# Performance work log

Hardware: AMD Instinct MI355X
Metric: run time of the kernel (lower is better)

## Reference

```python
import jax, jax.numpy as jnp
import numpy as np

N = 50000      # nodes
E = 800000     # edges (before self-loops)
F_IN = 128     # input features
HID = 64       # hidden width
CLS = 40       # classes
NEG_SLOPE = 0.2  # PyG GATConv default
EPS = 1e-16


def setup_inputs() -> dict:
    key = jax.random.key(0)
    ks = jax.random.split(key, 16)

    def lin(k, fi, fo):
        return jax.random.normal(k, (fi, fo), jnp.float32) / np.float32(np.sqrt(fi))

    def att(k, f):
        return jax.random.normal(k, (f,), jnp.float32) / np.float32(np.sqrt(f))

    return {
        "x": jax.random.normal(ks[0], (N, F_IN), jnp.float32),
        "edge_index": jax.random.randint(ks[1], (2, E), 0, N, dtype=jnp.int64),
        "W1": lin(ks[2], F_IN, HID), "a_src1": att(ks[3], HID), "a_dst1": att(ks[4], HID), "b1": jnp.zeros((HID,), jnp.float32),
        "W2": lin(ks[5], HID, HID),  "a_src2": att(ks[6], HID), "a_dst2": att(ks[7], HID), "b2": jnp.zeros((HID,), jnp.float32),
        "W3": lin(ks[8], HID, CLS),  "a_src3": att(ks[9], CLS), "a_dst3": att(ks[10], CLS), "b3": jnp.zeros((CLS,), jnp.float32),
    }


def gat_layer(x, src, dst, W, a_src, a_dst, b, n):
    # Single-head GATConv (PyG semantics, heads=1, add_self_loops already applied).
    h = x @ W                                  # [n, out]
    s_src = h @ a_src                          # [n]
    s_dst = h @ a_dst                          # [n]
    e = jax.nn.leaky_relu(s_src[src] + s_dst[dst], NEG_SLOPE)  # [E']
    # softmax over incoming edges of each destination node
    m = jax.ops.segment_max(e, dst, num_segments=n)            # [n]
    e = jnp.exp(e - m[dst])
    denom = jax.ops.segment_sum(e, dst, num_segments=n)        # [n]
    alpha = e / (denom[dst] + EPS)                             # [E']
    out = jax.ops.segment_sum(h[src] * alpha[:, None], dst, num_segments=n)
    return out + b


def reference(x, edge_index, W1, a_src1, a_dst1, b1, W2, a_src2, a_dst2, b2, W3, a_src3, a_dst3, b3):
    n = x.shape[0]
    loop = jnp.arange(n, dtype=edge_index.dtype)
    src = jnp.concatenate([edge_index[0], loop])   # add self-loops (GATConv default)
    dst = jnp.concatenate([edge_index[1], loop])

    h = gat_layer(x, src, dst, W1, a_src1, a_dst1, b1, n)
    h = jax.nn.gelu(h, approximate=False)          # torch F.gelu default = exact erf
    h = gat_layer(h, src, dst, W2, a_src2, a_dst2, b2, n)
    h = jax.nn.gelu(h, approximate=False)
    out = gat_layer(h, src, dst, W3, a_src3, a_dst3, b3, n)
    return out
```

## Files before the change

kernel.cpp:

```cpp
#include <hip/hip_runtime.h>
#include <hip/hip_bf16.h>
#include <math.h>


#define PAD_CAP 64
#define SCAT_BLOCKS 128

__device__ __forceinline__ int detect64(const int* __restrict__ ei) {
  int any = 0;
#pragma unroll
  for (int i = 1; i < 64; i += 2) any |= ei[i];
  return any == 0;
}

__device__ __forceinline__ void load_edge(const int* __restrict__ ei, int E,
                                          int e, int is64, int n, int& s,
                                          int& d) {
  if (is64) {
    s = ei[2 * e];
    d = ei[2 * (E + e)];
  } else {
    s = ei[e];
    d = ei[E + e];
  }
  s = min(max(s, 0), n - 1);
  d = min(max(d, 0), n - 1);
}


template <int F_IN, int F_OUT, bool SCATTER>
__global__ __launch_bounds__(256) void gemm_att(
    const float* __restrict__ x, const float* __restrict__ W,
    const float* __restrict__ a_src, const float* __restrict__ a_dst,
    __hip_bfloat16* __restrict__ h, float* __restrict__ s_src,
    float* __restrict__ s_dst, int n, const int* __restrict__ ei, int E,
    int* __restrict__ deg, int* __restrict__ col) {
  if constexpr (SCATTER) {
    if (blockIdx.x < SCAT_BLOCKS) {
      const int is64 = detect64(ei);
      const int total = E + n;
      const int stride = SCAT_BLOCKS * 256;
      int e = blockIdx.x * 256 + threadIdx.x;
      while (e < total) {
        int sv[8], dv[8], va[8], pos[8];
#pragma unroll
        for (int j = 0; j < 8; ++j) {
          const int ee = e + j * stride;
          va[j] = (ee < total);
          int s = 0, d = 0;
          if (va[j]) {
            if (ee < E) load_edge(ei, E, ee, is64, n, s, d);
            else { s = ee - E; d = ee - E; }
          }
          sv[j] = s;
          dv[j] = d;
        }
#pragma unroll
        for (int j = 0; j < 8; ++j)
          pos[j] = va[j] ? atomicAdd(deg + dv[j], 1) : PAD_CAP;
#pragma unroll
        for (int j = 0; j < 8; ++j)
          if (va[j] && pos[j] < PAD_CAP)
            col[((size_t)dv[j] << 6) + pos[j]] = sv[j];
        e += 8 * stride;
      }
      return;
    }
  }

  constexpr int TF = F_OUT / 4;
  __shared__ float Xt[F_IN * 65];
  __shared__ float red[2][4][64];
  const int wave = threadIdx.x >> 6, lane = threadIdx.x & 63;
  const int bid = SCATTER ? (int)blockIdx.x - SCAT_BLOCKS : (int)blockIdx.x;
  const int nb0 = bid * 64;
  const int node = nb0 + lane;

  {
    constexpr int Q = F_IN / 4;
    for (int i = threadIdx.x; i < 64 * Q; i += 256) {
      const int nd = i / Q, k4 = i % Q;
      float4 v = {0.f, 0.f, 0.f, 0.f};
      if (nb0 + nd < n)
        v = *(const float4*)(x + (size_t)(nb0 + nd) * F_IN + 4 * k4);
      Xt[(4 * k4 + 0) * 65 + nd] = v.x;
      Xt[(4 * k4 + 1) * 65 + nd] = v.y;
      Xt[(4 * k4 + 2) * 65 + nd] = v.z;
      Xt[(4 * k4 + 3) * 65 + nd] = v.w;
    }
  }
  __syncthreads();

  const int f0 = __builtin_amdgcn_readfirstlane(wave * TF);
  float acc[TF];
#pragma unroll
  for (int ff = 0; ff < TF; ++ff) acc[ff] = 0.f;

#pragma unroll 4
  for (int k = 0; k < F_IN; ++k) {
    const float xk = Xt[k * 65 + lane];
#pragma unroll
    for (int ff = 0; ff < TF; ++ff)
      acc[ff] = fmaf(xk, W[k * F_OUT + f0 + ff], acc[ff]);
  }

  float pa = 0.f, pb = 0.f;
#pragma unroll
  for (int ff = 0; ff < TF; ++ff) {
    pa = fmaf(acc[ff], a_src[f0 + ff], pa);
    pb = fmaf(acc[ff], a_dst[f0 + ff], pb);
  }
  if (node < n) {
#pragma unroll
    for (int ff = 0; ff < TF; ++ff)
      h[(size_t)node * F_OUT + f0 + ff] = __float2bfloat16(acc[ff]);
  }
  red[0][wave][lane] = pa;
  red[1][wave][lane] = pb;
  __syncthreads();
  if (wave == 0 && node < n) {
    s_src[node] = red[0][0][lane] + red[0][1][lane] + red[0][2][lane] +
                  red[0][3][lane];
    s_dst[node] = red[1][0][lane] + red[1][1][lane] + red[1][2][lane] +
                  red[1][3][lane];
  }
}

template <int F_OUT, bool GELU>
__global__ __launch_bounds__(256) void attn_aggr(
    const int* __restrict__ col, const int* __restrict__ deg_arr,
    const float* __restrict__ ssrc, const float* __restrict__ sdst,
    const __hip_bfloat16* __restrict__ h, const float* __restrict__ bias,
    float* __restrict__ out, int n) {
  constexpr int NF4 = (F_OUT + 3) / 4;
  const int wave = threadIdx.x >> 6, lane = threadIdx.x & 63;
  const int d = blockIdx.x * 4 + wave;
  if (d >= n) return;
  const int beg = d << 6;
  const int deg = min(deg_arr[d], PAD_CAP);
  const float sd = sdst[d];

  int s0 = 0;
  float w0 = 0.f;
  if (lane < deg) {
    s0 = col[beg + lane];
    float t = ssrc[s0] + sd;
    t = t > 0.f ? t : 0.2f * t;
    w0 = __expf(t);
  }
  float den = w0;
#pragma unroll
  for (int off = 32; off > 0; off >>= 1) den += __shfl_xor(den, off);
  const float inv = 1.f / (den + 1e-16f);

  const int q = lane >> 4, t4 = lane & 15;
  const bool act = (t4 < NF4);
  const unsigned short* __restrict__ hu = (const unsigned short*)h + 4 * t4;

  float ax = 0.f, ay = 0.f, az = 0.f, aw = 0.f;
  int i = 0;
  for (; i + 16 <= deg; i += 16) {
    int ss[4];
    float ww[4];
    uint2 hv[4];
#pragma unroll
    for (int j = 0; j < 4; ++j) {
      ss[j] = __shfl(s0, i + 4 * j + q);
      ww[j] = __shfl(w0, i + 4 * j + q);
    }
#pragma unroll
    for (int j = 0; j < 4; ++j) {
      hv[j].x = 0u;
      hv[j].y = 0u;
      if (act) hv[j] = *(const uint2*)(hu + (size_t)ss[j] * F_OUT);
    }
#pragma unroll
    for (int j = 0; j < 4; ++j) {
      ax = fmaf(ww[j], __uint_as_float(hv[j].x << 16), ax);
      ay = fmaf(ww[j], __uint_as_float(hv[j].x & 0xffff0000u), ay);
      az = fmaf(ww[j], __uint_as_float(hv[j].y << 16), az);
      aw = fmaf(ww[j], __uint_as_float(hv[j].y & 0xffff0000u), aw);
    }
  }
  for (; i < deg; i += 4) {
    const int ss = __shfl(s0, i + q);
    const float ww = __shfl(w0, i + q);
    uint2 hv;
    hv.x = 0u;
    hv.y = 0u;
    if (act) hv = *(const uint2*)(hu + (size_t)ss * F_OUT);
    ax = fmaf(ww, __uint_as_float(hv.x << 16), ax);
    ay = fmaf(ww, __uint_as_float(hv.x & 0xffff0000u), ay);
    az = fmaf(ww, __uint_as_float(hv.y << 16), az);
    aw = fmaf(ww, __uint_as_float(hv.y & 0xffff0000u), aw);
  }

#pragma unroll
  for (int off = 32; off >= 16; off >>= 1) {
    ax += __shfl_xor(ax, off);
    ay += __shfl_xor(ay, off);
    az += __shfl_xor(az, off);
    aw += __shfl_xor(aw, off);
  }

  if (lane < NF4) {
    const float4 bv = *(const float4*)(bias + 4 * lane);
    float r0 = ax * inv + bv.x;
    float r1 = ay * inv + bv.y;
    float r2 = az * inv + bv.z;
    float r3 = aw * inv + bv.w;
    if (GELU) {
      r0 = 0.5f * r0 * (1.f + erff(r0 * 0.70710678118654752f));
      r1 = 0.5f * r1 * (1.f + erff(r1 * 0.70710678118654752f));
      r2 = 0.5f * r2 * (1.f + erff(r2 * 0.70710678118654752f));
      r3 = 0.5f * r3 * (1.f + erff(r3 * 0.70710678118654752f));
    }
    *(float4*)(out + (size_t)d * F_OUT + 4 * lane) =
        make_float4(r0, r1, r2, r3);
  }
}

extern "C" void kernel_launch(void* const* d_in, const int* in_sizes, int n_in,
                              void* d_out, int out_size, void* d_ws,
                              size_t ws_size, hipStream_t stream) {
  const float* x = (const float*)d_in[0];
  const int* ei = (const int*)d_in[1];
  const float* W1 = (const float*)d_in[2];
  const float* as1 = (const float*)d_in[3];
  const float* ad1 = (const float*)d_in[4];
  const float* b1 = (const float*)d_in[5];
  const float* W2 = (const float*)d_in[6];
  const float* as2 = (const float*)d_in[7];
  const float* ad2 = (const float*)d_in[8];
  const float* b2 = (const float*)d_in[9];
  const float* W3 = (const float*)d_in[10];
  const float* as3 = (const float*)d_in[11];
  const float* ad3 = (const float*)d_in[12];
  const float* b3 = (const float*)d_in[13];

  const int n = in_sizes[0] / 128;
  const int E = in_sizes[1] / 2;

  const size_t need = ((size_t)n * (32 + 64 + 1 + 1 + 1 + PAD_CAP)) * 4 + 256;
  if (ws_size < need) return;

  __hip_bfloat16* hb = (__hip_bfloat16*)d_ws;
  float* B = (float*)d_ws + (size_t)n * 32;
  float* ssrc = B + (size_t)n * 64;
  float* sdst = ssrc + n;
  int* deg = (int*)(sdst + n);
  int* col = deg + n;

  const int gemm_blocks = (n + 63) / 64;
  const int aggr_blocks = (n + 3) / 4;

  hipMemsetAsync(deg, 0, (size_t)n * 4, stream);
  gemm_att<128, 64, true><<<gemm_blocks + SCAT_BLOCKS, 256, 0, stream>>>(
      x, W1, as1, ad1, hb, ssrc, sdst, n, ei, E, deg, col);
  attn_aggr<64, true><<<aggr_blocks, 256, 0, stream>>>(col, deg, ssrc, sdst,
                                                       hb, b1, B, n);

  gemm_att<64, 64, false><<<gemm_blocks, 256, 0, stream>>>(
      B, W2, as2, ad2, hb, ssrc, sdst, n, nullptr, 0, nullptr, nullptr);
  attn_aggr<64, true><<<aggr_blocks, 256, 0, stream>>>(col, deg, ssrc, sdst,
                                                       hb, b2, B, n);

  gemm_att<64, 40, false><<<gemm_blocks, 256, 0, stream>>>(
      B, W3, as3, ad3, hb, ssrc, sdst, n, nullptr, 0, nullptr, nullptr);
  attn_aggr<40, false><<<aggr_blocks, 256, 0, stream>>>(
      col, deg, ssrc, sdst, hb, b3, (float*)d_out, n);
}
```

Before: 252.9 us.

## Fuse attention aggregation with next layer's GEMM into one kernel

Adds an aggr_gemm kernel that runs the softmax-weighted neighbor aggregation plus bias and GELU for 64 destination nodes, stages the result in shared memory, then multiplies by the next layer's weights and computes the attention scores. This replaces separate attn_aggr and gemm_att launches for layers 1→2 and 2→3, removing the fp32 intermediate buffer round-trip through global memory and two launches. Ping-pong bf16 and score buffers avoid read/write hazards. The cost is 1024-thread blocks where each wave handles four nodes serially, which may reduce latency hiding for the gather, and the GEMM phase leaves some waves idle for F_OUT=40.

```diff
diff --git a/kernel.cpp b/kernel.cpp
--- a/kernel.cpp
+++ b/kernel.cpp
@@ -123,6 +123,144 @@
                   red[0][3][lane];
     s_dst[node] = red[1][0][lane] + red[1][1][lane] + red[1][2][lane] +
                   red[1][3][lane];
+  }
+}
+
+template <int F_OUT>
+__global__ __launch_bounds__(1024) void aggr_gemm(
+    const int* __restrict__ col, const int* __restrict__ deg_arr,
+    const float* __restrict__ ssrc, const float* __restrict__ sdst,
+    const __hip_bfloat16* __restrict__ h_in, const float* __restrict__ bias_in,
+    const float* __restrict__ W, const float* __restrict__ a_src,
+    const float* __restrict__ a_dst, __hip_bfloat16* __restrict__ h_out,
+    float* __restrict__ ssrc_out, float* __restrict__ sdst_out, int n) {
+  constexpr int F_IN = 64;
+  constexpr int NW = F_OUT / 4;
+  __shared__ float Xt[F_IN * 65];
+  __shared__ float red[2][16][64];
+  const int wave = threadIdx.x >> 6, lane = threadIdx.x & 63;
+  const int q = lane >> 4, t4 = lane & 15;
+  const int nb0 = blockIdx.x * 64;
+
+  float4 bv = make_float4(0.f, 0.f, 0.f, 0.f);
+  if (lane < 16) bv = *(const float4*)(bias_in + 4 * lane);
+
+  const unsigned short* __restrict__ hu = (const unsigned short*)h_in + 4 * t4;
+
+  for (int r = 0; r < 4; ++r) {
+    const int dl = 4 * wave + r;
+    const int d = nb0 + dl;
+    float ax = 0.f, ay = 0.f, az = 0.f, aw_ = 0.f, inv = 0.f;
+    if (d < n) {
+      const int beg = d << 6;
+      const int deg = min(deg_arr[d], PAD_CAP);
+      const float sd = sdst[d];
+      int s0 = 0;
+      float w0 = 0.f;
+      if (lane < deg) {
+        s0 = col[beg + lane];
+        float t = ssrc[s0] + sd;
+        t = t > 0.f ? t : 0.2f * t;
+        w0 = __expf(t);
+      }
+      float den = w0;
+#pragma unroll
+      for (int off = 32; off > 0; off >>= 1) den += __shfl_xor(den, off);
+      inv = 1.f / (den + 1e-16f);
+
+      int i = 0;
+      for (; i + 16 <= deg; i += 16) {
+        int ss[4];
+        float ww[4];
+        uint2 hv[4];
+#pragma unroll
+        for (int j = 0; j < 4; ++j) {
+          ss[j] = __shfl(s0, i + 4 * j + q);
+          ww[j] = __shfl(w0, i + 4 * j + q);
+        }
+#pragma unroll
+        for (int j = 0; j < 4; ++j)
+          hv[j] = *(const uint2*)(hu + (size_t)ss[j] * F_IN);
+#pragma unroll
+        for (int j = 0; j < 4; ++j) {
+          ax = fmaf(ww[j], __uint_as_float(hv[j].x << 16), ax);
+          ay = fmaf(ww[j], __uint_as_float(hv[j].x & 0xffff0000u), ay);
+          az = fmaf(ww[j], __uint_as_float(hv[j].y << 16), az);
+          aw_ = fmaf(ww[j], __uint_as_float(hv[j].y & 0xffff0000u), aw_);
+        }
+      }
+      for (; i < deg; i += 4) {
+        const int ss = __shfl(s0, i + q);
+        const float ww = __shfl(w0, i + q);
+        const uint2 hv = *(const uint2*)(hu + (size_t)ss * F_IN);
+        ax = fmaf(ww, __uint_as_float(hv.x << 16), ax);
+        ay = fmaf(ww, __uint_as_float(hv.x & 0xffff0000u), ay);
+        az = fmaf(ww, __uint_as_float(hv.y << 16), az);
+        aw_ = fmaf(ww, __uint_as_float(hv.y & 0xffff0000u), aw_);
+      }
+#pragma unroll
+      for (int off = 32; off >= 16; off >>= 1) {
+        ax += __shfl_xor(ax, off);
+        ay += __shfl_xor(ay, off);
+        az += __shfl_xor(az, off);
+        aw_ += __shfl_xor(aw_, off);
+      }
+    }
+    if (lane < 16) {
+      float r0 = 0.f, r1 = 0.f, r2 = 0.f, r3 = 0.f;
+      if (d < n) {
+        r0 = ax * inv + bv.x;
+        r1 = ay * inv + bv.y;
+        r2 = az * inv + bv.z;
+        r3 = aw_ * inv + bv.w;
+        r0 = 0.5f * r0 * (1.f + erff(r0 * 0.70710678118654752f));
+        r1 = 0.5f * r1 * (1.f + erff(r1 * 0.70710678118654752f));
+        r2 = 0.5f * r2 * (1.f + erff(r2 * 0.70710678118654752f));
+        r3 = 0.5f * r3 * (1.f + erff(r3 * 0.70710678118654752f));
+      }
+      Xt[(4 * lane + 0) * 65 + dl] = r0;
+      Xt[(4 * lane + 1) * 65 + dl] = r1;
+      Xt[(4 * lane + 2) * 65 + dl] = r2;
+      Xt[(4 * lane + 3) * 65 + dl] = r3;
+    }
+  }
+  __syncthreads();
+
+  float pa = 0.f, pb = 0.f;
+  const int node = nb0 + lane;
+  if (wave < NW) {
+    const int f0 = __builtin_amdgcn_readfirstlane(wave * 4);
+    float acc[4] = {0.f, 0.f, 0.f, 0.f};
+#pragma unroll 4
+    for (int k = 0; k < F_IN; ++k) {
+      const float xk = Xt[k * 65 + lane];
+#pragma unroll
+      for (int ff = 0; ff < 4; ++ff)
+        acc[ff] = fmaf(xk, W[k * F_OUT + f0 + ff], acc[ff]);
+    }
+#pragma unroll
+    for (int ff = 0; ff < 4; ++ff) {
+      pa = fmaf(acc[ff], a_src[f0 + ff], pa);
+      pb = fmaf(acc[ff], a_dst[f0 + ff], pb);
+    }
+    if (node < n) {
+#pragma unroll
+      for (int ff = 0; ff < 4; ++ff)
+        h_out[(size_t)node * F_OUT + f0 + ff] = __float2bfloat16(acc[ff]);
+    }
+  }
+  red[0][wave][lane] = pa;
+  red[1][wave][lane] = pb;
+  __syncthreads();
+  if (wave == 0 && node < n) {
+    float sa = 0.f, sb = 0.f;
+#pragma unroll
+    for (int w = 0; w < NW; ++w) {
+      sa += red[0][w][lane];
+      sb += red[1][w][lane];
+    }
+    ssrc_out[node] = sa;
+    sdst_out[node] = sb;
   }
 }
 
@@ -241,14 +379,16 @@
   const int n = in_sizes[0] / 128;
   const int E = in_sizes[1] / 2;
 
-  const size_t need = ((size_t)n * (32 + 64 + 1 + 1 + 1 + PAD_CAP)) * 4 + 256;
+  const size_t need = ((size_t)n * (32 + 32 + 1 + 1 + 1 + 1 + 1 + PAD_CAP)) * 4 + 256;
   if (ws_size < need) return;
 
-  __hip_bfloat16* hb = (__hip_bfloat16*)d_ws;
-  float* B = (float*)d_ws + (size_t)n * 32;
-  float* ssrc = B + (size_t)n * 64;
-  float* sdst = ssrc + n;
-  int* deg = (int*)(sdst + n);
+  __hip_bfloat16* hbA = (__hip_bfloat16*)d_ws;
+  __hip_bfloat16* hbB = hbA + (size_t)n * 64;
+  float* ssrcA = (float*)d_ws + (size_t)n * 64;
+  float* sdstA = ssrcA + n;
+  float* ssrcB = sdstA + n;
+  float* sdstB = ssrcB + n;
+  int* deg = (int*)(sdstB + n);
   int* col = deg + n;
 
   const int gemm_blocks = (n + 63) / 64;
@@ -256,17 +396,14 @@
 
   hipMemsetAsync(deg, 0, (size_t)n * 4, stream);
   gemm_att<128, 64, true><<<gemm_blocks + SCAT_BLOCKS, 256, 0, stream>>>(
-      x, W1, as1, ad1, hb, ssrc, sdst, n, ei, E, deg, col);
-  attn_aggr<64, true><<<aggr_blocks, 256, 0, stream>>>(col, deg, ssrc, sdst,
-                                                       hb, b1, B, n);
-
-  gemm_att<64, 64, false><<<gemm_blocks, 256, 0, stream>>>(
-      B, W2, as2, ad2, hb, ssrc, sdst, n, nullptr, 0, nullptr, nullptr);
-  attn_aggr<64, true><<<aggr_blocks, 256, 0, stream>>>(col, deg, ssrc, sdst,
-                                                       hb, b2, B, n);
-
-  gemm_att<64, 40, false><<<gemm_blocks, 256, 0, stream>>>(
-      B, W3, as3, ad3, hb, ssrc, sdst, n, nullptr, 0, nullptr, nullptr);
+      x, W1, as1, ad1, hbA, ssrcA, sdstA, n, ei, E, deg, col);
+
+  aggr_gemm<64><<<gemm_blocks, 1024, 0, stream>>>(
+      col, deg, ssrcA, sdstA, hbA, b1, W2, as2, ad2, hbB, ssrcB, sdstB, n);
+
+  aggr_gemm<40><<<gemm_blocks, 1024, 0, stream>>>(
+      col, deg, ssrcB, sdstB, hbB, b2, W3, as3, ad3, hbA, ssrcA, sdstA, n);
+
   attn_aggr<40, false><<<aggr_blocks, 256, 0, stream>>>(
-      col, deg, ssrc, sdst, hb, b3, (float*)d_out, n);
-}
+      col, deg, ssrcA, sdstA, hbA, b3, (float*)d_out, n);
+}
```

After: 247.8 us. 2.0% less time.

## Slice hidden features into 8-wide planes and split aggregation per slice

Applied to the files above, without the earlier changes.

Hidden activations are stored as feature-sliced planes of 8 bf16 values per node. Each aggregation block now handles a single slice for 4 destination nodes, so the random gathers touch a much smaller per-slice working set that can stay resident in cache. Adjacency columns are stored as 16-bit indices, halving CSR traffic, and bf16 packing is done manually with vector stores. The cost is that each slice recomputes the softmax weights, multiplying col and score gathers by the slice count. The grid is also 8x larger, the gather loop always walks all 64 padded slots, and 16-bit indices only work while n is at most 65536.

```diff
diff --git a/kernel.cpp b/kernel.cpp
--- a/kernel.cpp
+++ b/kernel.cpp
@@ -27,53 +27,56 @@
   d = min(max(d, 0), n - 1);
 }
 
-
-template <int F_IN, int F_OUT, bool SCATTER>
-__global__ __launch_bounds__(256) void gemm_att(
+__device__ __forceinline__ unsigned bfbits(float a) {
+  unsigned u = __float_as_uint(a);
+  return (u + 0x7fffu + ((u >> 16) & 1u)) >> 16;
+}
+__device__ __forceinline__ unsigned pk2(float a, float b) {
+  return bfbits(a) | (bfbits(b) << 16);
+}
+
+__global__ __launch_bounds__(256) void k1_gemm(
     const float* __restrict__ x, const float* __restrict__ W,
     const float* __restrict__ a_src, const float* __restrict__ a_dst,
-    __hip_bfloat16* __restrict__ h, float* __restrict__ s_src,
+    unsigned short* __restrict__ hs, float* __restrict__ s_src,
     float* __restrict__ s_dst, int n, const int* __restrict__ ei, int E,
-    int* __restrict__ deg, int* __restrict__ col) {
-  if constexpr (SCATTER) {
-    if (blockIdx.x < SCAT_BLOCKS) {
-      const int is64 = detect64(ei);
-      const int total = E + n;
-      const int stride = SCAT_BLOCKS * 256;
-      int e = blockIdx.x * 256 + threadIdx.x;
-      while (e < total) {
-        int sv[8], dv[8], va[8], pos[8];
-#pragma unroll
-        for (int j = 0; j < 8; ++j) {
-          const int ee = e + j * stride;
-          va[j] = (ee < total);
-          int s = 0, d = 0;
-          if (va[j]) {
-            if (ee < E) load_edge(ei, E, ee, is64, n, s, d);
-            else { s = ee - E; d = ee - E; }
-          }
-          sv[j] = s;
-          dv[j] = d;
+    int* __restrict__ deg, unsigned short* __restrict__ col) {
+  constexpr int F_IN = 128, F_OUT = 64;
+  if (blockIdx.x < SCAT_BLOCKS) {
+    const int is64 = detect64(ei);
+    const int total = E + n;
+    const int stride = SCAT_BLOCKS * 256;
+    int e = blockIdx.x * 256 + threadIdx.x;
+    while (e < total) {
+      int sv[8], dv[8], va[8], pos[8];
+#pragma unroll
+      for (int j = 0; j < 8; ++j) {
+        const int ee = e + j * stride;
+        va[j] = (ee < total);
+        int s = 0, d = 0;
+        if (va[j]) {
+          if (ee < E) load_edge(ei, E, ee, is64, n, s, d);
+          else { s = ee - E; d = ee - E; }
         }
-#pragma unroll
-        for (int j = 0; j < 8; ++j)
-          pos[j] = va[j] ? atomicAdd(deg + dv[j], 1) : PAD_CAP;
-#pragma unroll
-        for (int j = 0; j < 8; ++j)
-          if (va[j] && pos[j] < PAD_CAP)
-            col[((size_t)dv[j] << 6) + pos[j]] = sv[j];
-        e += 8 * stride;
+        sv[j] = s;
+        dv[j] = d;
       }
-      return;
-    }
-  }
-
-  constexpr int TF = F_OUT / 4;
+#pragma unroll
+      for (int j = 0; j < 8; ++j)
+        pos[j] = va[j] ? atomicAdd(deg + dv[j], 1) : PAD_CAP;
+#pragma unroll
+      for (int j = 0; j < 8; ++j)
+        if (va[j] && pos[j] < PAD_CAP)
+          col[((size_t)dv[j] << 6) + pos[j]] = (unsigned short)sv[j];
+      e += 8 * stride;
+    }
+    return;
+  }
+
   __shared__ float Xt[F_IN * 65];
   __shared__ float red[2][4][64];
   const int wave = threadIdx.x >> 6, lane = threadIdx.x & 63;
-  const int bid = SCATTER ? (int)blockIdx.x - SCAT_BLOCKS : (int)blockIdx.x;
-  const int nb0 = bid * 64;
+  const int nb0 = ((int)blockIdx.x - SCAT_BLOCKS) * 64;
   const int node = nb0 + lane;
 
   {
@@ -91,29 +94,31 @@
   }
   __syncthreads();
 
-  const int f0 = __builtin_amdgcn_readfirstlane(wave * TF);
-  float acc[TF];
-#pragma unroll
-  for (int ff = 0; ff < TF; ++ff) acc[ff] = 0.f;
-
+  const int f0 = __builtin_amdgcn_readfirstlane(wave * 16);
+  float acc[16];
+#pragma unroll
+  for (int ff = 0; ff < 16; ++ff) acc[ff] = 0.f;
 #pragma unroll 4
   for (int k = 0; k < F_IN; ++k) {
     const float xk = Xt[k * 65 + lane];
 #pragma unroll
-    for (int ff = 0; ff < TF; ++ff)
+    for (int ff = 0; ff < 16; ++ff)
       acc[ff] = fmaf(xk, W[k * F_OUT + f0 + ff], acc[ff]);
   }
-
   float pa = 0.f, pb = 0.f;
 #pragma unroll
-  for (int ff = 0; ff < TF; ++ff) {
+  for (int ff = 0; ff < 16; ++ff) {
     pa = fmaf(acc[ff], a_src[f0 + ff], pa);
     pb = fmaf(acc[ff], a_dst[f0 + ff], pb);
   }
   if (node < n) {
-#pragma unroll
-    for (int ff = 0; ff < TF; ++ff)
-      h[(size_t)node * F_OUT + f0 + ff] = __float2bfloat16(acc[ff]);
+    uint4 u0, u1;
+    u0.x = pk2(acc[0], acc[1]);  u0.y = pk2(acc[2], acc[3]);
+    u0.z = pk2(acc[4], acc[5]);  u0.w = pk2(acc[6], acc[7]);
+    u1.x = pk2(acc[8], acc[9]);  u1.y = pk2(acc[10], acc[11]);
+    u1.z = pk2(acc[12], acc[13]); u1.w = pk2(acc[14], acc[15]);
+    *(uint4*)(hs + ((size_t)(2 * wave) * n + node) * 8) = u0;
+    *(uint4*)(hs + ((size_t)(2 * wave + 1) * n + node) * 8) = u1;
   }
   red[0][wave][lane] = pa;
   red[1][wave][lane] = pb;
@@ -126,25 +131,104 @@
   }
 }
 
-template <int F_OUT, bool GELU>
-__global__ __launch_bounds__(256) void attn_aggr(
-    const int* __restrict__ col, const int* __restrict__ deg_arr,
+template <int F_OUT>
+__global__ __launch_bounds__(256) void gemm_slice(
+    const float* __restrict__ aggS, const float* __restrict__ W,
+    const float* __restrict__ a_src, const float* __restrict__ a_dst,
+    unsigned short* __restrict__ hs, float* __restrict__ s_src,
+    float* __restrict__ s_dst, int n) {
+  constexpr int F_IN = 64;
+  __shared__ float Xt[F_IN * 65];
+  __shared__ float red[2][4][64];
+  const int wave = threadIdx.x >> 6, lane = threadIdx.x & 63;
+  const int nb0 = blockIdx.x * 64;
+  const int node = nb0 + lane;
+
+#pragma unroll
+  for (int t = 0; t < 4; ++t) {
+    const int idx = t * 256 + threadIdx.x;
+    const int nd = idx & 63, c = idx >> 6;
+    const int sl = c >> 1, off = (c & 1) << 2;
+    float4 v = {0.f, 0.f, 0.f, 0.f};
+    if (nb0 + nd < n)
+      v = *(const float4*)(aggS + ((size_t)sl * n + nb0 + nd) * 8 + off);
+    const int f = sl * 8 + off;
+    Xt[(f + 0) * 65 + nd] = v.x;
+    Xt[(f + 1) * 65 + nd] = v.y;
+    Xt[(f + 2) * 65 + nd] = v.z;
+    Xt[(f + 3) * 65 + nd] = v.w;
+  }
+  __syncthreads();
+
+  const int f0 = __builtin_amdgcn_readfirstlane(wave * 16);
+  int fcl[16];
+#pragma unroll
+  for (int ff = 0; ff < 16; ++ff) fcl[ff] = min(f0 + ff, F_OUT - 1);
+  float acc[16];
+#pragma unroll
+  for (int ff = 0; ff < 16; ++ff) acc[ff] = 0.f;
+#pragma unroll 4
+  for (int k = 0; k < F_IN; ++k) {
+    const float xk = Xt[k * 65 + lane];
+#pragma unroll
+    for (int ff = 0; ff < 16; ++ff)
+      acc[ff] = fmaf(xk, W[k * F_OUT + fcl[ff]], acc[ff]);
+  }
+#pragma unroll
+  for (int ff = 0; ff < 16; ++ff)
+    if (f0 + ff >= F_OUT) acc[ff] = 0.f;
+  float pa = 0.f, pb = 0.f;
+#pragma unroll
+  for (int ff = 0; ff < 16; ++ff) {
+    pa = fmaf(acc[ff], a_src[fcl[ff]], pa);
+    pb = fmaf(acc[ff], a_dst[fcl[ff]], pb);
+  }
+  if (node < n) {
+    if (2 * wave * 8 < F_OUT) {
+      uint4 u;
+      u.x = pk2(acc[0], acc[1]); u.y = pk2(acc[2], acc[3]);
+      u.z = pk2(acc[4], acc[5]); u.w = pk2(acc[6], acc[7]);
+      *(uint4*)(hs + ((size_t)(2 * wave) * n + node) * 8) = u;
+    }
+    if ((2 * wave + 1) * 8 < F_OUT) {
+      uint4 u;
+      u.x = pk2(acc[8], acc[9]);  u.y = pk2(acc[10], acc[11]);
+      u.z = pk2(acc[12], acc[13]); u.w = pk2(acc[14], acc[15]);
+      *(uint4*)(hs + ((size_t)(2 * wave + 1) * n + node) * 8) = u;
+    }
+  }
+  red[0][wave][lane] = pa;
+  red[1][wave][lane] = pb;
+  __syncthreads();
+  if (wave == 0 && node < n) {
+    s_src[node] = red[0][0][lane] + red[0][1][lane] + red[0][2][lane] +
+                  red[0][3][lane];
+    s_dst[node] = red[1][0][lane] + red[1][1][lane] + red[1][2][lane] +
+                  red[1][3][lane];
+  }
+}
+
+template <bool GELU, bool FINAL>
+__global__ __launch_bounds__(256) void aggr_slice(
+    const unsigned short* __restrict__ col, const int* __restrict__ deg_arr,
     const float* __restrict__ ssrc, const float* __restrict__ sdst,
-    const __hip_bfloat16* __restrict__ h, const float* __restrict__ bias,
-    float* __restrict__ out, int n) {
-  constexpr int NF4 = (F_OUT + 3) / 4;
+    const unsigned short* __restrict__ hs, const float* __restrict__ bias,
+    float* __restrict__ outp, int n) {
+  const int slice = blockIdx.x & 7;
+  constexpr int NS = FINAL ? 5 : 8;
+  if (slice >= NS) return;
   const int wave = threadIdx.x >> 6, lane = threadIdx.x & 63;
-  const int d = blockIdx.x * 4 + wave;
+  const int d = (blockIdx.x >> 3) * 4 + wave;
   if (d >= n) return;
-  const int beg = d << 6;
+
   const int deg = min(deg_arr[d], PAD_CAP);
   const float sd = sdst[d];
-
   int s0 = 0;
+  if (lane < deg) s0 = col[((size_t)d << 6) + lane];
+  const float sval = (lane < deg) ? ssrc[s0] : 0.f;
   float w0 = 0.f;
   if (lane < deg) {
-    s0 = col[beg + lane];
-    float t = ssrc[s0] + sd;
+    float t = sval + sd;
     t = t > 0.f ? t : 0.2f * t;
     w0 = __expf(t);
   }
@@ -153,70 +237,37 @@
   for (int off = 32; off > 0; off >>= 1) den += __shfl_xor(den, off);
   const float inv = 1.f / (den + 1e-16f);
 
-  const int q = lane >> 4, t4 = lane & 15;
-  const bool act = (t4 < NF4);
-  const unsigned short* __restrict__ hu = (const unsigned short*)h + 4 * t4;
-
-  float ax = 0.f, ay = 0.f, az = 0.f, aw = 0.f;
-  int i = 0;
-  for (; i + 16 <= deg; i += 16) {
-    int ss[4];
-    float ww[4];
-    uint2 hv[4];
-#pragma unroll
-    for (int j = 0; j < 4; ++j) {
-      ss[j] = __shfl(s0, i + 4 * j + q);
-      ww[j] = __shfl(w0, i + 4 * j + q);
-    }
-#pragma unroll
-    for (int j = 0; j < 4; ++j) {
-      hv[j].x = 0u;
-      hv[j].y = 0u;
-      if (act) hv[j] = *(const uint2*)(hu + (size_t)ss[j] * F_OUT);
-    }
-#pragma unroll
-    for (int j = 0; j < 4; ++j) {
-      ax = fmaf(ww[j], __uint_as_float(hv[j].x << 16), ax);
-      ay = fmaf(ww[j], __uint_as_float(hv[j].x & 0xffff0000u), ay);
-      az = fmaf(ww[j], __uint_as_float(hv[j].y << 16), az);
-      aw = fmaf(ww[j], __uint_as_float(hv[j].y & 0xffff0000u), aw);
-    }
-  }
-  for (; i < deg; i += 4) {
-    const int ss = __shfl(s0, i + q);
-    const float ww = __shfl(w0, i + q);
-    uint2 hv;
-    hv.x = 0u;
-    hv.y = 0u;
-    if (act) hv = *(const uint2*)(hu + (size_t)ss * F_OUT);
-    ax = fmaf(ww, __uint_as_float(hv.x << 16), ax);
-    ay = fmaf(ww, __uint_as_float(hv.x & 0xffff0000u), ay);
-    az = fmaf(ww, __uint_as_float(hv.y << 16), az);
-    aw = fmaf(ww, __uint_as_float(hv.y & 0xffff0000u), aw);
-  }
-
-#pragma unroll
-  for (int off = 32; off >= 16; off >>= 1) {
-    ax += __shfl_xor(ax, off);
-    ay += __shfl_xor(ay, off);
-    az += __shfl_xor(az, off);
-    aw += __shfl_xor(aw, off);
-  }
-
-  if (lane < NF4) {
-    const float4 bv = *(const float4*)(bias + 4 * lane);
-    float r0 = ax * inv + bv.x;
-    float r1 = ay * inv + bv.y;
-    float r2 = az * inv + bv.z;
-    float r3 = aw * inv + bv.w;
+  const unsigned* __restrict__ hp =
+      (const unsigned*)hs + ((size_t)slice * n) * 4;
+  const int sub = lane >> 2, b = lane & 3;
+  float a0 = 0.f, a1 = 0.f;
+#pragma unroll
+  for (int t = 0; t < 4; ++t) {
+    const int es = 16 * t + sub;
+    const int ss = __shfl(s0, es);
+    const float ww = __shfl(w0, es);
+    const unsigned v = hp[((size_t)ss << 2) | b];
+    a0 = fmaf(ww, __uint_as_float(v << 16), a0);
+    a1 = fmaf(ww, __uint_as_float(v & 0xffff0000u), a1);
+  }
+#pragma unroll
+  for (int off = 4; off <= 32; off <<= 1) {
+    a0 += __shfl_xor(a0, off);
+    a1 += __shfl_xor(a1, off);
+  }
+  if (lane < 4) {
+    const int f = slice * 8 + 2 * lane;
+    float r0 = a0 * inv + bias[f];
+    float r1 = a1 * inv + bias[f + 1];
     if (GELU) {
       r0 = 0.5f * r0 * (1.f + erff(r0 * 0.70710678118654752f));
       r1 = 0.5f * r1 * (1.f + erff(r1 * 0.70710678118654752f));
-      r2 = 0.5f * r2 * (1.f + erff(r2 * 0.70710678118654752f));
-      r3 = 0.5f * r3 * (1.f + erff(r3 * 0.70710678118654752f));
-    }
-    *(float4*)(out + (size_t)d * F_OUT + 4 * lane) =
-        make_float4(r0, r1, r2, r3);
+    }
+    if (FINAL)
+      *(float2*)(outp + (size_t)d * 40 + f) = make_float2(r0, r1);
+    else
+      *(float2*)(outp + (((size_t)slice * n + d) << 3) + 2 * lane) =
+          make_float2(r0, r1);
   }
 }
 
@@ -241,32 +292,36 @@
   const int n = in_sizes[0] / 128;
   const int E = in_sizes[1] / 2;
 
-  const size_t need = ((size_t)n * (32 + 64 + 1 + 1 + 1 + PAD_CAP)) * 4 + 256;
+  const size_t need = ((size_t)n * (32 + 64 + 1 + 1 + 1 + 32)) * 4 + 256;
   if (ws_size < need) return;
 
-  __hip_bfloat16* hb = (__hip_bfloat16*)d_ws;
-  float* B = (float*)d_ws + (size_t)n * 32;
-  float* ssrc = B + (size_t)n * 64;
+  unsigned short* hs = (unsigned short*)d_ws;
+  float* aggS = (float*)d_ws + (size_t)n * 32;
+  float* ssrc = aggS + (size_t)n * 64;
   float* sdst = ssrc + n;
   int* deg = (int*)(sdst + n);
-  int* col = deg + n;
+  unsigned short* col = (unsigned short*)(deg + n);
 
   const int gemm_blocks = (n + 63) / 64;
-  const int aggr_blocks = (n + 3) / 4;
+  const int aggr_blocks = ((n + 3) / 4) * 8;
 
   hipMemsetAsync(deg, 0, (size_t)n * 4, stream);
-  gemm_att<128, 64, true><<<gemm_blocks + SCAT_BLOCKS, 256, 0, stream>>>(
-      x, W1, as1, ad1, hb, ssrc, sdst, n, ei, E, deg, col);
-  attn_aggr<64, true><<<aggr_blocks, 256, 0, stream>>>(col, deg, ssrc, sdst,
-                                                       hb, b1, B, n);
-
-  gemm_att<64, 64, false><<<gemm_blocks, 256, 0, stream>>>(
-      B, W2, as2, ad2, hb, ssrc, sdst, n, nullptr, 0, nullptr, nullptr);
-  attn_aggr<64, true><<<aggr_blocks, 256, 0, stream>>>(col, deg, ssrc, sdst,
-                                                       hb, b2, B, n);
-
-  gemm_att<64, 40, false><<<gemm_blocks, 256, 0, stream>>>(
-      B, W3, as3, ad3, hb, ssrc, sdst, n, nullptr, 0, nullptr, nullptr);
-  attn_aggr<40, false><<<aggr_blocks, 256, 0, stream>>>(
-      col, deg, ssrc, sdst, hb, b3, (float*)d_out, n);
-}
+
+  k1_gemm<<<gemm_blocks + SCAT_BLOCKS, 256, 0, stream>>>(
+      x, W1, as1, ad1, hs, ssrc, sdst, n, ei, E, deg, col);
+
+  aggr_slice<true, false><<<aggr_blocks, 256, 0, stream>>>(
+      col, deg, ssrc, sdst, hs, b1, aggS, n);
+
+  gemm_slice<64><<<gemm_blocks, 256, 0, stream>>>(aggS, W2, as2, ad2, hs,
+                                                  ssrc, sdst, n);
+
+  aggr_slice<true, false><<<aggr_blocks, 256, 0, stream>>>(
+      col, deg, ssrc, sdst, hs, b2, aggS, n);
+
+  gemm_slice<40><<<gemm_blocks, 256, 0, stream>>>(aggS, W3, as3, ad3, hs,
+                                                  ssrc, sdst, n);
+
+  aggr_slice<false, true><<<aggr_blocks, 256, 0, stream>>>(
+      col, deg, ssrc, sdst, hs, b3, (float*)d_out, n);
+}
```

After: 556.3 us. +120.0%, slower.
